# Kernel tuning notes

Hardware: AMD Instinct MI355X
Metric: run time of the kernel (lower is better)

Reference implementation:

```python
import jax, jax.numpy as jnp
import numpy as np

N = 20000   # nodes
E = 320000  # edges (before self-loops)
HID = 64    # hidden_dim
H = 4       # attention heads
C = HID     # per-head channels (concat=False -> mean over heads)
CDIM = 8    # contrastive_dim
NEG_SLOPE = 0.2


def setup_inputs() -> dict:
    key = jax.random.key(0)
    ks = jax.random.split(key, 32)
    g = lambda k, shape: (jax.random.normal(k, shape, jnp.float32) * 0.05)
    inp = {
        "x": jax.random.normal(ks[0], (N, 8), jnp.float32),
        "edge_index": jax.random.randint(ks[1], (2, E), 0, N, jnp.int64),
        # lc_encode MLP: 8 -> 32 -> HID
        "W_enc1": g(ks[2], (8, 32)),  "b_enc1": jnp.zeros((32,), jnp.float32),
        "W_enc2": g(ks[3], (32, HID)), "b_enc2": jnp.zeros((HID,), jnp.float32),
        # three GATConv layers: lin (HID -> H*C, no bias), att_src/att_dst (H, C), bias (C,)
        "W_g1": g(ks[4], (HID, H * C)), "as1": g(ks[5], (H, C)), "ad1": g(ks[6], (H, C)), "bg1": jnp.zeros((C,), jnp.float32),
        "W_g2": g(ks[7], (HID, H * C)), "as2": g(ks[8], (H, C)), "ad2": g(ks[9], (H, C)), "bg2": jnp.zeros((C,), jnp.float32),
        "W_g3": g(ks[10], (HID, H * C)), "as3": g(ks[11], (H, C)), "ad3": g(ks[12], (H, C)), "bg3": jnp.zeros((C,), jnp.float32),
        # output MLP: HID -> 64 -> 32 -> CDIM (dropout inactive at eval)
        "W_o1": g(ks[13], (HID, 64)), "b_o1": jnp.zeros((64,), jnp.float32),
        "W_o2": g(ks[14], (64, 32)),  "b_o2": jnp.zeros((32,), jnp.float32),
        "W_o3": g(ks[15], (32, CDIM)), "b_o3": jnp.zeros((CDIM,), jnp.float32),
    }
    return inp


def gat_conv(x, src, dst, n, W, att_src, att_dst, bias):
    # PyG GATConv, heads=H, concat=False (mean over heads), eval mode (no dropout)
    h = (x @ W).reshape(n, H, C)                       # [N,H,C]
    a_src = jnp.einsum('nhc,hc->nh', h, att_src)        # [N,H]
    a_dst = jnp.einsum('nhc,hc->nh', h, att_dst)        # [N,H]
    logits = jax.nn.leaky_relu(a_src[src] + a_dst[dst], NEG_SLOPE)  # [Etot,H]
    m = jax.ops.segment_max(logits, dst, num_segments=n)            # segment softmax (stable)
    e = jnp.exp(logits - m[dst])
    denom = jax.ops.segment_sum(e, dst, num_segments=n)
    alpha = e / (denom[dst] + 1e-16)                    # [Etot,H]
    msg = h[src] * alpha[:, :, None]                    # [Etot,H,C]
    out = jax.ops.segment_sum(msg, dst, num_segments=n) # [N,H,C]
    return out.mean(axis=1) + bias                      # concat=False -> head mean


def reference(x, edge_index, W_enc1, b_enc1, W_enc2, b_enc2,
              W_g1, as1, ad1, bg1, W_g2, as2, ad2, bg2, W_g3, as3, ad3, bg3,
              W_o1, b_o1, W_o2, b_o2, W_o3, b_o3):
    n = x.shape[0]
    loops = jnp.arange(n, dtype=edge_index.dtype)       # GATConv add_self_loops=True
    src = jnp.concatenate([edge_index[0], loops])
    dst = jnp.concatenate([edge_index[1], loops])

    h = jax.nn.elu(jax.nn.elu(x @ W_enc1 + b_enc1) @ W_enc2 + b_enc2)
    h1 = gat_conv(h, src, dst, n, W_g1, as1, ad1, bg1) + h
    h2 = gat_conv(h1, src, dst, n, W_g2, as2, ad2, bg2) + h1
    h3 = gat_conv(h2, src, dst, n, W_g3, as3, ad3, bg3) + h2

    o = jax.nn.elu(h3 @ W_o1 + b_o1)
    o = jax.nn.elu(o @ W_o2 + b_o2)
    return o @ W_o3 + b_o3
```

## Files before the change

### kernel.cpp

```cpp
#include <hip/hip_runtime.h>
#include <cstdint>
#include <cstddef>

#define NEG_SLOPE 0.2f

__device__ __forceinline__ float elu_f(float x) {
    return x > 0.f ? x : expm1f(x);
}

__global__ __launch_bounds__(256) void encoder_kernel(
    const float* __restrict__ x,
    const float* __restrict__ W1, const float* __restrict__ b1,
    const float* __restrict__ W2, const float* __restrict__ b2,
    const float* __restrict__ vfold0,
    float* __restrict__ h0, float* __restrict__ asrc, float* __restrict__ adst,
    int n_nodes) {
    __shared__ float vsd[512];
    const int t = threadIdx.x;
    if (t < 128) *(float4*)(vsd + t * 4) = *(const float4*)(vfold0 + t * 4);
    __syncthreads();
    const int i = blockIdx.x * blockDim.x + t;
    if (i >= n_nodes) return;
    const float4* xp = (const float4*)(x + (size_t)i * 8);
    float4 x0 = xp[0], x1 = xp[1];
    float xi[8] = {x0.x, x0.y, x0.z, x0.w, x1.x, x1.y, x1.z, x1.w};
    float h1[32];
#pragma unroll
    for (int j = 0; j < 32; ++j) {
        float a = b1[j];
#pragma unroll
        for (int k = 0; k < 8; ++k) a += xi[k] * W1[k * 32 + j];
        h1[j] = elu_f(a);
    }
    float* dst = h0 + (size_t)i * 64;
    float adot[8];
#pragma unroll
    for (int jj = 0; jj < 8; ++jj) adot[jj] = 0.f;
    for (int j = 0; j < 64; ++j) {
        float a = b2[j];
#pragma unroll
        for (int k = 0; k < 32; ++k) a += h1[k] * W2[k * 64 + j];
        a = elu_f(a);
        dst[j] = a;
#pragma unroll
        for (int jj = 0; jj < 8; ++jj) adot[jj] += a * vsd[j * 8 + jj];
    }
#pragma unroll
    for (int h = 0; h < 4; ++h) {
        asrc[i * 4 + h] = adot[h];
        adst[i * 4 + h] = adot[4 + h];
    }
}

__global__ void zero_detect_kernel(const int* __restrict__ ei, int* __restrict__ cnt,
                                   int* __restrict__ flag, int n) {
    int i = blockIdx.x * blockDim.x + threadIdx.x;
    if (i < n) cnt[i] = 0;
    if (i == 0) {
        int acc = 0;
#pragma unroll
        for (int k = 0; k < 8; ++k) acc |= ei[2 * k + 1];
        flag[0] = (acc == 0) ? 1 : 0;
    }
}

__global__ void count_kernel(const int* __restrict__ ei, const int* __restrict__ flag,
                             int E, int Etot, int* __restrict__ cnt) {
    int e = blockIdx.x * blockDim.x + threadIdx.x;
    if (e >= Etot) return;
    int d;
    if (e < E) d = flag[0] ? ei[2 * (size_t)(E + e)] : ei[E + e];
    else       d = e - E;
    atomicAdd(&cnt[d], 1);
}

#define SCAN_B 256
__global__ void scan1_kernel(const int* __restrict__ cnt, int* __restrict__ incl,
                             int* __restrict__ bsum, int n) {
    __shared__ int sd[SCAN_B];
    int t = threadIdx.x;
    int g = blockIdx.x * SCAN_B + t;
    int v = (g < n) ? cnt[g] : 0;
    sd[t] = v;
    __syncthreads();
    for (int off = 1; off < SCAN_B; off <<= 1) {
        int add = (t >= off) ? sd[t - off] : 0;
        __syncthreads();
        sd[t] += add;
        __syncthreads();
    }
    if (g < n) incl[g] = sd[t];
    if (t == SCAN_B - 1) bsum[blockIdx.x] = sd[SCAN_B - 1];
}

__global__ void scan2_kernel(const int* __restrict__ bsum, int* __restrict__ boff, int nb) {
    __shared__ int sd[256];
    int t = threadIdx.x;
    int v = (t < nb) ? bsum[t] : 0;
    sd[t] = v;
    __syncthreads();
    for (int off = 1; off < 256; off <<= 1) {
        int add = (t >= off) ? sd[t - off] : 0;
        __syncthreads();
        sd[t] += add;
        __syncthreads();
    }
    if (t < nb) boff[t] = sd[t] - v;
}

__global__ void scan3_kernel(const int* __restrict__ incl, const int* __restrict__ boff,
                             const int* __restrict__ cnt, int* __restrict__ rowptr,
                             int* __restrict__ cursor, int n) {
    int i = blockIdx.x * SCAN_B + threadIdx.x;
    if (i >= n) return;
    int e = incl[i] + boff[blockIdx.x];
    rowptr[i + 1] = e;
    cursor[i] = e - cnt[i];
    if (i == 0) rowptr[0] = 0;
}

__global__ void fill_kernel(const int* __restrict__ ei, const int* __restrict__ flag,
                            int E, int Etot, int* __restrict__ cursor,
                            int* __restrict__ col) {
    int e = blockIdx.x * blockDim.x + threadIdx.x;
    if (e >= Etot) return;
    int s, d;
    if (e < E) {
        if (flag[0]) { s = ei[2 * (size_t)e]; d = ei[2 * (size_t)(E + e)]; }
        else         { s = ei[e];             d = ei[E + e]; }
    } else {
        s = d = e - E;
    }
    int pos = atomicAdd(&cursor[d], 1);
    col[pos] = s;
}

__global__ __launch_bounds__(256) void fold_all_kernel(
    const float* __restrict__ W0, const float* __restrict__ as0, const float* __restrict__ ad0,
    const float* __restrict__ W1, const float* __restrict__ as1, const float* __restrict__ ad1,
    const float* __restrict__ W2, const float* __restrict__ as2, const float* __restrict__ ad2,
    float* __restrict__ vfold) {
    const int l = blockIdx.x;
    const float* W   = (l == 0) ? W0  : (l == 1) ? W1  : W2;
    const float* as_ = (l == 0) ? as0 : (l == 1) ? as1 : as2;
    const float* ad_ = (l == 0) ? ad0 : (l == 1) ? ad1 : ad2;
    const int t = threadIdx.x;
#pragma unroll
    for (int u = 0; u < 2; ++u) {
        const int e = t * 2 + u;
        const int k = e >> 3, j = e & 7, h = j & 3;
        const float* av = (j < 4) ? as_ : ad_;
        float s = 0.f;
        const float* wr = W + k * 256 + h * 64;
        const float* ar = av + h * 64;
#pragma unroll 8
        for (int cc = 0; cc < 64; ++cc) s += wr[cc] * ar[cc];
        vfold[l * 512 + k * 8 + j] = s;
    }
}

__global__ __launch_bounds__(256) void gat_agg_kernel(
    const float* __restrict__ bin, const float* __restrict__ asrc,
    const float* __restrict__ adst, const int* __restrict__ rowptr,
    const int* __restrict__ col, float* __restrict__ g, int n_nodes) {
    const int grp = threadIdx.x >> 4;
    const int q = threadIdx.x & 15;
    const int n = blockIdx.x * 16 + grp;
    if (n >= n_nodes) return;
    const float4 ad4 = *(const float4*)(adst + (size_t)n * 4);
    const int start = rowptr[n], end = rowptr[n + 1];

    float acc[4][4];
#pragma unroll
    for (int h = 0; h < 4; ++h)
#pragma unroll
        for (int z = 0; z < 4; ++z) acc[h][z] = 0.f;
    float4 den4 = make_float4(0.f, 0.f, 0.f, 0.f);

    for (int base = start; base < end; base += 16) {
        const int cnt = min(16, end - base);
        int c = 0;
        float4 w4 = make_float4(0.f, 0.f, 0.f, 0.f);
        if (base + q < end) {
            c = col[base + q];
            const float4 av = *(const float4*)(asrc + (size_t)c * 4);
            float l0 = av.x + ad4.x; l0 = l0 > 0.f ? l0 : NEG_SLOPE * l0;
            float l1 = av.y + ad4.y; l1 = l1 > 0.f ? l1 : NEG_SLOPE * l1;
            float l2 = av.z + ad4.z; l2 = l2 > 0.f ? l2 : NEG_SLOPE * l2;
            float l3 = av.w + ad4.w; l3 = l3 > 0.f ? l3 : NEG_SLOPE * l3;
            w4.x = __expf(fminf(l0, 60.f));
            w4.y = __expf(fminf(l1, 60.f));
            w4.z = __expf(fminf(l2, 60.f));
            w4.w = __expf(fminf(l3, 60.f));
            den4.x += w4.x; den4.y += w4.y; den4.z += w4.z; den4.w += w4.w;
        }
        int j = 0;
        for (; j + 4 <= cnt; j += 4) {
#pragma unroll
            for (int u = 0; u < 4; ++u) {
                const int s = __shfl(c, j + u, 16);
                const float4 hv = *(const float4*)(bin + (size_t)s * 64 + q * 4);
                const float wx = __shfl(w4.x, j + u, 16);
                const float wy = __shfl(w4.y, j + u, 16);
                const float wz = __shfl(w4.z, j + u, 16);
                const float ww = __shfl(w4.w, j + u, 16);
                acc[0][0] += wx * hv.x; acc[0][1] += wx * hv.y;
                acc[0][2] += wx * hv.z; acc[0][3] += wx * hv.w;
                acc[1][0] += wy * hv.x; acc[1][1] += wy * hv.y;
                acc[1][2] += wy * hv.z; acc[1][3] += wy * hv.w;
                acc[2][0] += wz * hv.x; acc[2][1] += wz * hv.y;
                acc[2][2] += wz * hv.z; acc[2][3] += wz * hv.w;
                acc[3][0] += ww * hv.x; acc[3][1] += ww * hv.y;
                acc[3][2] += ww * hv.z; acc[3][3] += ww * hv.w;
            }
        }
        for (; j < cnt; ++j) {
            const int s = __shfl(c, j, 16);
            const float4 hv = *(const float4*)(bin + (size_t)s * 64 + q * 4);
            const float wx = __shfl(w4.x, j, 16);
            const float wy = __shfl(w4.y, j, 16);
            const float wz = __shfl(w4.z, j, 16);
            const float ww = __shfl(w4.w, j, 16);
            acc[0][0] += wx * hv.x; acc[0][1] += wx * hv.y;
            acc[0][2] += wx * hv.z; acc[0][3] += wx * hv.w;
            acc[1][0] += wy * hv.x; acc[1][1] += wy * hv.y;
            acc[1][2] += wy * hv.z; acc[1][3] += wy * hv.w;
            acc[2][0] += wz * hv.x; acc[2][1] += wz * hv.y;
            acc[2][2] += wz * hv.z; acc[2][3] += wz * hv.w;
            acc[3][0] += ww * hv.x; acc[3][1] += ww * hv.y;
            acc[3][2] += ww * hv.z; acc[3][3] += ww * hv.w;
        }
    }
#pragma unroll
    for (int off = 1; off < 16; off <<= 1) {
        den4.x += __shfl_xor(den4.x, off, 16);
        den4.y += __shfl_xor(den4.y, off, 16);
        den4.z += __shfl_xor(den4.z, off, 16);
        den4.w += __shfl_xor(den4.w, off, 16);
    }
    const float i0 = 1.f / (den4.x + 1e-16f);
    const float i1 = 1.f / (den4.y + 1e-16f);
    const float i2 = 1.f / (den4.z + 1e-16f);
    const float i3 = 1.f / (den4.w + 1e-16f);
    float* gr = g + (size_t)n * 256 + q * 4;
    *(float4*)(gr +   0) = make_float4(acc[0][0]*i0, acc[0][1]*i0, acc[0][2]*i0, acc[0][3]*i0);
    *(float4*)(gr +  64) = make_float4(acc[1][0]*i1, acc[1][1]*i1, acc[1][2]*i1, acc[1][3]*i1);
    *(float4*)(gr + 128) = make_float4(acc[2][0]*i2, acc[2][1]*i2, acc[2][2]*i2, acc[2][3]*i2);
    *(float4*)(gr + 192) = make_float4(acc[3][0]*i3, acc[3][1]*i3, acc[3][2]*i3, acc[3][3]*i3);
}

#define GSTR 132
__global__ __launch_bounds__(256) void gat_post_kernel(
    const float* __restrict__ g, const float* __restrict__ W,
    const float* __restrict__ bias, const float* __restrict__ xin,
    const float* __restrict__ vfold_next, int has_next,
    float* __restrict__ out, float* __restrict__ asrc, float* __restrict__ adst,
    int n_nodes) {
    __shared__ float gS[64 * GSTR];
    __shared__ float Wp[128 * 64];
    __shared__ float vN[512];
    const int t = threadIdx.x;
    const int n0 = blockIdx.x * 64;
    const int cg = t & 7;
    const int ng = t >> 3;

    if (has_next && t < 128) *(float4*)(vN + t * 4) = *(const float4*)(vfold_next + t * 4);

    float acc[2][8];
#pragma unroll
    for (int i = 0; i < 2; ++i)
#pragma unroll
        for (int qq = 0; qq < 8; ++qq) acc[i][qq] = 0.f;

    for (int slab = 0; slab < 2; ++slab) {
        __syncthreads();
#pragma unroll
        for (int j = 0; j < 8; ++j) {
            const int idx = j * 256 + t;
            const int nl = idx >> 5;
            const int c4 = idx & 31;
            float4 v = make_float4(0.f, 0.f, 0.f, 0.f);
            if (n0 + nl < n_nodes)
                v = *(const float4*)(g + (size_t)(n0 + nl) * 256 + slab * 128 + c4 * 4);
            *(float4*)(gS + nl * GSTR + c4 * 4) = v;
        }
#pragma unroll
        for (int j = 0; j < 8; ++j) {
            const int f4 = j * 256 + t;
            const int kl = f4 >> 4;
            const int kap = slab * 128 + kl;
            const int h = kap >> 6, kk = kap & 63;
            const int c = (f4 & 15) * 4;
            *(float4*)(Wp + kl * 64 + c) = *(const float4*)(W + kk * 256 + h * 64 + c);
        }
        __syncthreads();
#pragma unroll 4
        for (int kl = 0; kl < 128; ++kl) {
            const float a0 = gS[(ng * 2 + 0) * GSTR + kl];
            const float a1 = gS[(ng * 2 + 1) * GSTR + kl];
            const float4 b0 = *(const float4*)(Wp + kl * 64 + cg * 8);
            const float4 b1 = *(const float4*)(Wp + kl * 64 + cg * 8 + 4);
            acc[0][0] += a0 * b0.x; acc[0][1] += a0 * b0.y;
            acc[0][2] += a0 * b0.z; acc[0][3] += a0 * b0.w;
            acc[0][4] += a0 * b1.x; acc[0][5] += a0 * b1.y;
            acc[0][6] += a0 * b1.z; acc[0][7] += a0 * b1.w;
            acc[1][0] += a1 * b0.x; acc[1][1] += a1 * b0.y;
            acc[1][2] += a1 * b0.z; acc[1][3] += a1 * b0.w;
            acc[1][4] += a1 * b1.x; acc[1][5] += a1 * b1.y;
            acc[1][6] += a1 * b1.z; acc[1][7] += a1 * b1.w;
        }
    }

    const int c0 = cg * 8;
    const float4 bb0 = *(const float4*)(bias + c0);
    const float4 bb1 = *(const float4*)(bias + c0 + 4);
    float o[2][8];
#pragma unroll
    for (int i = 0; i < 2; ++i) {
        const int n = n0 + ng * 2 + i;
        if (n < n_nodes) {
            const float4 x0 = *(const float4*)(xin + (size_t)n * 64 + c0);
            const float4 x1 = *(const float4*)(xin + (size_t)n * 64 + c0 + 4);
            o[i][0] = 0.25f * acc[i][0] + bb0.x + x0.x;
            o[i][1] = 0.25f * acc[i][1] + bb0.y + x0.y;
            o[i][2] = 0.25f * acc[i][2] + bb0.z + x0.z;
            o[i][3] = 0.25f * acc[i][3] + bb0.w + x0.w;
            o[i][4] = 0.25f * acc[i][4] + bb1.x + x1.x;
            o[i][5] = 0.25f * acc[i][5] + bb1.y + x1.y;
            o[i][6] = 0.25f * acc[i][6] + bb1.z + x1.z;
            o[i][7] = 0.25f * acc[i][7] + bb1.w + x1.w;
            *(float4*)(out + (size_t)n * 64 + c0) =
                make_float4(o[i][0], o[i][1], o[i][2], o[i][3]);
            *(float4*)(out + (size_t)n * 64 + c0 + 4) =
                make_float4(o[i][4], o[i][5], o[i][6], o[i][7]);
        } else {
#pragma unroll
            for (int qq = 0; qq < 8; ++qq) o[i][qq] = 0.f;
        }
    }

    if (has_next) {
        float pj[2][8];
#pragma unroll
        for (int i = 0; i < 2; ++i)
#pragma unroll
            for (int jj = 0; jj < 8; ++jj) pj[i][jj] = 0.f;
#pragma unroll
        for (int cidx = 0; cidx < 8; ++cidx) {
#pragma unroll
            for (int jj = 0; jj < 8; ++jj) {
                const float vv = vN[(c0 + cidx) * 8 + jj];
                pj[0][jj] += o[0][cidx] * vv;
                pj[1][jj] += o[1][cidx] * vv;
            }
        }
#pragma unroll
        for (int off = 1; off < 8; off <<= 1) {
#pragma unroll
            for (int i = 0; i < 2; ++i)
#pragma unroll
                for (int jj = 0; jj < 8; ++jj)
                    pj[i][jj] += __shfl_xor(pj[i][jj], off);
        }
        if (cg == 0) {
#pragma unroll
            for (int i = 0; i < 2; ++i) {
                const int n = n0 + ng * 2 + i;
                if (n < n_nodes) {
#pragma unroll
                    for (int h = 0; h < 4; ++h) {
                        asrc[n * 4 + h] = pj[i][h];
                        adst[n * 4 + h] = pj[i][4 + h];
                    }
                }
            }
        }
    }
}

__global__ __launch_bounds__(256) void out_mlp_kernel(
    const float* __restrict__ h, const float* __restrict__ W1,
    const float* __restrict__ b1, const float* __restrict__ W2,
    const float* __restrict__ b2, const float* __restrict__ W3,
    const float* __restrict__ b3, float* __restrict__ out, int n_nodes) {
    const int wid = threadIdx.x >> 6;
    const int lane = threadIdx.x & 63;
    const int n = blockIdx.x * 4 + wid;
    if (n >= n_nodes) return;
    const float hv = h[(size_t)n * 64 + lane];
    float a = b1[lane];
#pragma unroll
    for (int k = 0; k < 64; ++k) a += __shfl(hv, k) * W1[k * 64 + lane];
    const float o1 = elu_f(a);
    const int c2 = lane & 31;
    float a2 = b2[c2];
#pragma unroll
    for (int k = 0; k < 64; ++k) a2 += __shfl(o1, k) * W2[k * 32 + c2];
    const float o2 = elu_f(a2);
    const int c3 = lane & 7;
    float a3 = b3[c3];
#pragma unroll
    for (int k = 0; k < 32; ++k) a3 += __shfl(o2, k) * W3[k * 8 + c3];
    if (lane < 8) out[(size_t)n * 8 + lane] = a3;
}

extern "C" void kernel_launch(void* const* d_in, const int* in_sizes, int n_in,
                              void* d_out, int out_size, void* d_ws, size_t ws_size,
                              hipStream_t stream) {
    const float* x     = (const float*)d_in[0];
    const int*   ei    = (const int*)d_in[1];
    const float* Wenc1 = (const float*)d_in[2];
    const float* benc1 = (const float*)d_in[3];
    const float* Wenc2 = (const float*)d_in[4];
    const float* benc2 = (const float*)d_in[5];
    const float* Wg[3]  = {(const float*)d_in[6],  (const float*)d_in[10], (const float*)d_in[14]};
    const float* as_[3] = {(const float*)d_in[7],  (const float*)d_in[11], (const float*)d_in[15]};
    const float* ad_[3] = {(const float*)d_in[8],  (const float*)d_in[12], (const float*)d_in[16]};
    const float* bg[3]  = {(const float*)d_in[9],  (const float*)d_in[13], (const float*)d_in[17]};
    const float* Wo1 = (const float*)d_in[18];
    const float* bo1 = (const float*)d_in[19];
    const float* Wo2 = (const float*)d_in[20];
    const float* bo2 = (const float*)d_in[21];
    const float* Wo3 = (const float*)d_in[22];
    const float* bo3 = (const float*)d_in[23];

    const int N = in_sizes[0] / 8;
    const int E = in_sizes[1] / 2;
    const int Etot = E + N;
    const int nblk = (N + SCAN_B - 1) / SCAN_B;

    float* buf0  = (float*)d_ws;
    float* buf1  = buf0 + (size_t)N * 64;
    float* g     = buf1 + (size_t)N * 64;
    float* asrc  = g + (size_t)N * 256;
    float* adst  = asrc + (size_t)N * 4;
    float* vfold = adst + (size_t)N * 4;
    int* rowptr = (int*)(vfold + 3 * 512);
    int* cursor = rowptr + (N + 2);
    int* cnt    = cursor + N;
    int* incl   = cnt + N;
    int* bsum   = incl + N;
    int* boff   = bsum + 256;
    int* flag   = boff + 256;
    int* col    = flag + 2;

    zero_detect_kernel<<<(N + 255) / 256, 256, 0, stream>>>(ei, cnt, flag, N);
    count_kernel<<<(Etot + 255) / 256, 256, 0, stream>>>(ei, flag, E, Etot, cnt);
    scan1_kernel<<<nblk, SCAN_B, 0, stream>>>(cnt, incl, bsum, N);
    scan2_kernel<<<1, 256, 0, stream>>>(bsum, boff, nblk);
    scan3_kernel<<<nblk, SCAN_B, 0, stream>>>(incl, boff, cnt, rowptr, cursor, N);
    fill_kernel<<<(Etot + 255) / 256, 256, 0, stream>>>(ei, flag, E, Etot, cursor, col);

    fold_all_kernel<<<3, 256, 0, stream>>>(Wg[0], as_[0], ad_[0],
                                           Wg[1], as_[1], ad_[1],
                                           Wg[2], as_[2], ad_[2], vfold);

    encoder_kernel<<<(N + 255) / 256, 256, 0, stream>>>(x, Wenc1, benc1, Wenc2, benc2,
                                                        vfold, buf0, asrc, adst, N);

    float* bin = buf0;
    float* bout = buf1;
    for (int l = 0; l < 3; ++l) {
        gat_agg_kernel<<<(N + 15) / 16, 256, 0, stream>>>(bin, asrc, adst, rowptr, col,
                                                          g, N);
        const int has_next = (l < 2) ? 1 : 0;
        gat_post_kernel<<<(N + 63) / 64, 256, 0, stream>>>(
            g, Wg[l], bg[l], bin, vfold + (l + 1 < 3 ? (l + 1) * 512 : 0), has_next,
            bout, asrc, adst, N);
        float* tmp = bin; bin = bout; bout = tmp;
    }

    out_mlp_kernel<<<(N + 3) / 4, 256, 0, stream>>>(bin, Wo1, bo1, Wo2, bo2, Wo3, bo3,
                                                    (float*)d_out, N);
}
```

Before: 339.2 us.

## Fuse prep kernels, use single-pass decoupled scan, fold output MLP into last GAT

Merges the zeroing/flag detection and weight folding into one prep kernel, and replaces the three-kernel block scan with a single-pass scan where each block spins on earlier blocks' published sums. It also fuses the output MLP into the final gat_post kernel, so the last layer's node features stay in shared memory and are not written out and read back. The goal is fewer launches and less global traffic. The one-pass scan assumes all earlier blocks make progress (79 blocks, fine on this GPU) and caps the block count at 128.

```diff
diff --git a/kernel.cpp b/kernel.cpp
--- a/kernel.cpp
+++ b/kernel.cpp
@@ -8,60 +8,42 @@
     return x > 0.f ? x : expm1f(x);
 }
 
-__global__ __launch_bounds__(256) void encoder_kernel(
-    const float* __restrict__ x,
-    const float* __restrict__ W1, const float* __restrict__ b1,
-    const float* __restrict__ W2, const float* __restrict__ b2,
-    const float* __restrict__ vfold0,
-    float* __restrict__ h0, float* __restrict__ asrc, float* __restrict__ adst,
-    int n_nodes) {
-    __shared__ float vsd[512];
-    const int t = threadIdx.x;
-    if (t < 128) *(float4*)(vsd + t * 4) = *(const float4*)(vfold0 + t * 4);
-    __syncthreads();
-    const int i = blockIdx.x * blockDim.x + t;
-    if (i >= n_nodes) return;
-    const float4* xp = (const float4*)(x + (size_t)i * 8);
-    float4 x0 = xp[0], x1 = xp[1];
-    float xi[8] = {x0.x, x0.y, x0.z, x0.w, x1.x, x1.y, x1.z, x1.w};
-    float h1[32];
-#pragma unroll
-    for (int j = 0; j < 32; ++j) {
-        float a = b1[j];
-#pragma unroll
-        for (int k = 0; k < 8; ++k) a += xi[k] * W1[k * 32 + j];
-        h1[j] = elu_f(a);
-    }
-    float* dst = h0 + (size_t)i * 64;
-    float adot[8];
-#pragma unroll
-    for (int jj = 0; jj < 8; ++jj) adot[jj] = 0.f;
-    for (int j = 0; j < 64; ++j) {
-        float a = b2[j];
-#pragma unroll
-        for (int k = 0; k < 32; ++k) a += h1[k] * W2[k * 64 + j];
-        a = elu_f(a);
-        dst[j] = a;
-#pragma unroll
-        for (int jj = 0; jj < 8; ++jj) adot[jj] += a * vsd[j * 8 + jj];
-    }
-#pragma unroll
-    for (int h = 0; h < 4; ++h) {
-        asrc[i * 4 + h] = adot[h];
-        adst[i * 4 + h] = adot[4 + h];
-    }
-}
-
-__global__ void zero_detect_kernel(const int* __restrict__ ei, int* __restrict__ cnt,
-                                   int* __restrict__ flag, int n) {
-    int i = blockIdx.x * blockDim.x + threadIdx.x;
-    if (i < n) cnt[i] = 0;
-    if (i == 0) {
-        int acc = 0;
-#pragma unroll
-        for (int k = 0; k < 8; ++k) acc |= ei[2 * k + 1];
-        flag[0] = (acc == 0) ? 1 : 0;
-    }
+__global__ __launch_bounds__(256) void prep_kernel(
+    const int* __restrict__ ei,
+    const float* __restrict__ W0, const float* __restrict__ as0, const float* __restrict__ ad0,
+    const float* __restrict__ W1, const float* __restrict__ as1, const float* __restrict__ ad1,
+    const float* __restrict__ W2, const float* __restrict__ as2, const float* __restrict__ ad2,
+    int* __restrict__ cnt, int* __restrict__ ready, int* __restrict__ flag,
+    float* __restrict__ vfold, int n) {
+    const int b = blockIdx.x, t = threadIdx.x;
+    if (b < 79) {
+        const int i = b * 256 + t;
+        if (i < n) cnt[i] = 0;
+        if (b == 0) {
+            if (t < 128) ready[t] = 0;
+            if (t == 0) {
+                int acc = 0;
+#pragma unroll
+                for (int k = 0; k < 8; ++k) acc |= ei[2 * k + 1];
+                flag[0] = (acc == 0) ? 1 : 0;
+            }
+        }
+        return;
+    }
+    const int e = (b - 79) * 256 + t;
+    if (e >= 1536) return;
+    const int l = e >> 9, rem = e & 511;
+    const int k = rem >> 3, j = rem & 7, h = j & 3;
+    const float* W   = (l == 0) ? W0  : (l == 1) ? W1  : W2;
+    const float* as_ = (l == 0) ? as0 : (l == 1) ? as1 : as2;
+    const float* ad_ = (l == 0) ? ad0 : (l == 1) ? ad1 : ad2;
+    const float* av = (j < 4) ? as_ : ad_;
+    const float* wr = W + k * 256 + h * 64;
+    const float* ar = av + h * 64;
+    float s = 0.f;
+#pragma unroll 8
+    for (int cc = 0; cc < 64; ++cc) s += wr[cc] * ar[cc];
+    vfold[l * 512 + k * 8 + j] = s;
 }
 
 __global__ void count_kernel(const int* __restrict__ ei, const int* __restrict__ flag,
@@ -75,12 +57,15 @@
 }
 
 #define SCAN_B 256
-__global__ void scan1_kernel(const int* __restrict__ cnt, int* __restrict__ incl,
-                             int* __restrict__ bsum, int n) {
+__global__ __launch_bounds__(256) void scan_onepass_kernel(
+    const int* __restrict__ cnt, int* __restrict__ ready,
+    int* __restrict__ rowptr, int* __restrict__ cursor, int n) {
     __shared__ int sd[SCAN_B];
-    int t = threadIdx.x;
-    int g = blockIdx.x * SCAN_B + t;
-    int v = (g < n) ? cnt[g] : 0;
+    __shared__ int sred[128];
+    __shared__ int s_pref;
+    const int b = blockIdx.x, t = threadIdx.x;
+    const int g = b * SCAN_B + t;
+    const int v = (g < n) ? cnt[g] : 0;
     sd[t] = v;
     __syncthreads();
     for (int off = 1; off < SCAN_B; off <<= 1) {
@@ -89,34 +74,30 @@
         sd[t] += add;
         __syncthreads();
     }
-    if (g < n) incl[g] = sd[t];
-    if (t == SCAN_B - 1) bsum[blockIdx.x] = sd[SCAN_B - 1];
-}
-
-__global__ void scan2_kernel(const int* __restrict__ bsum, int* __restrict__ boff, int nb) {
-    __shared__ int sd[256];
-    int t = threadIdx.x;
-    int v = (t < nb) ? bsum[t] : 0;
-    sd[t] = v;
-    __syncthreads();
-    for (int off = 1; off < 256; off <<= 1) {
-        int add = (t >= off) ? sd[t - off] : 0;
-        __syncthreads();
-        sd[t] += add;
-        __syncthreads();
-    }
-    if (t < nb) boff[t] = sd[t] - v;
-}
-
-__global__ void scan3_kernel(const int* __restrict__ incl, const int* __restrict__ boff,
-                             const int* __restrict__ cnt, int* __restrict__ rowptr,
-                             int* __restrict__ cursor, int n) {
-    int i = blockIdx.x * SCAN_B + threadIdx.x;
-    if (i >= n) return;
-    int e = incl[i] + boff[blockIdx.x];
-    rowptr[i + 1] = e;
-    cursor[i] = e - cnt[i];
-    if (i == 0) rowptr[0] = 0;
+    if (t == SCAN_B - 1) atomicExch(&ready[b], sd[SCAN_B - 1] + 1);
+    if (t < 128) {
+        int pv = 0;
+        if (t < b) {
+            do { pv = atomicAdd(&ready[t], 0); __builtin_amdgcn_s_sleep(1); } while (pv == 0);
+            pv -= 1;
+        }
+        sred[t] = pv;
+    }
+    __syncthreads();
+    if (t == 0) {
+        int s = 0;
+#pragma unroll 8
+        for (int i = 0; i < 128; ++i) s += sred[i];
+        s_pref = s;
+    }
+    __syncthreads();
+    const int pre = s_pref;
+    if (g < n) {
+        const int e = pre + sd[t];
+        rowptr[g + 1] = e;
+        cursor[g] = e - v;
+        if (g == 0) rowptr[0] = 0;
+    }
 }
 
 __global__ void fill_kernel(const int* __restrict__ ei, const int* __restrict__ flag,
@@ -135,27 +116,47 @@
     col[pos] = s;
 }
 
-__global__ __launch_bounds__(256) void fold_all_kernel(
-    const float* __restrict__ W0, const float* __restrict__ as0, const float* __restrict__ ad0,
-    const float* __restrict__ W1, const float* __restrict__ as1, const float* __restrict__ ad1,
-    const float* __restrict__ W2, const float* __restrict__ as2, const float* __restrict__ ad2,
-    float* __restrict__ vfold) {
-    const int l = blockIdx.x;
-    const float* W   = (l == 0) ? W0  : (l == 1) ? W1  : W2;
-    const float* as_ = (l == 0) ? as0 : (l == 1) ? as1 : as2;
-    const float* ad_ = (l == 0) ? ad0 : (l == 1) ? ad1 : ad2;
+__global__ __launch_bounds__(256) void encoder_kernel(
+    const float* __restrict__ x,
+    const float* __restrict__ W1, const float* __restrict__ b1,
+    const float* __restrict__ W2, const float* __restrict__ b2,
+    const float* __restrict__ vfold0,
+    float* __restrict__ h0, float* __restrict__ asrc, float* __restrict__ adst,
+    int n_nodes) {
+    __shared__ float vsd[512];
     const int t = threadIdx.x;
-#pragma unroll
-    for (int u = 0; u < 2; ++u) {
-        const int e = t * 2 + u;
-        const int k = e >> 3, j = e & 7, h = j & 3;
-        const float* av = (j < 4) ? as_ : ad_;
-        float s = 0.f;
-        const float* wr = W + k * 256 + h * 64;
-        const float* ar = av + h * 64;
-#pragma unroll 8
-        for (int cc = 0; cc < 64; ++cc) s += wr[cc] * ar[cc];
-        vfold[l * 512 + k * 8 + j] = s;
+    if (t < 128) *(float4*)(vsd + t * 4) = *(const float4*)(vfold0 + t * 4);
+    __syncthreads();
+    const int i = blockIdx.x * blockDim.x + t;
+    if (i >= n_nodes) return;
+    const float4* xp = (const float4*)(x + (size_t)i * 8);
+    float4 x0 = xp[0], x1 = xp[1];
+    float xi[8] = {x0.x, x0.y, x0.z, x0.w, x1.x, x1.y, x1.z, x1.w};
+    float h1[32];
+#pragma unroll
+    for (int j = 0; j < 32; ++j) {
+        float a = b1[j];
+#pragma unroll
+        for (int k = 0; k < 8; ++k) a += xi[k] * W1[k * 32 + j];
+        h1[j] = elu_f(a);
+    }
+    float* dst = h0 + (size_t)i * 64;
+    float adot[8];
+#pragma unroll
+    for (int jj = 0; jj < 8; ++jj) adot[jj] = 0.f;
+    for (int j = 0; j < 64; ++j) {
+        float a = b2[j];
+#pragma unroll
+        for (int k = 0; k < 32; ++k) a += h1[k] * W2[k * 64 + j];
+        a = elu_f(a);
+        dst[j] = a;
+#pragma unroll
+        for (int jj = 0; jj < 8; ++jj) adot[jj] += a * vsd[j * 8 + jj];
+    }
+#pragma unroll
+    for (int h = 0; h < 4; ++h) {
+        asrc[i * 4 + h] = adot[h];
+        adst[i * 4 + h] = adot[4 + h];
     }
 }
 
@@ -255,7 +256,10 @@
     const float* __restrict__ bias, const float* __restrict__ xin,
     const float* __restrict__ vfold_next, int has_next,
     float* __restrict__ out, float* __restrict__ asrc, float* __restrict__ adst,
-    int n_nodes) {
+    const float* __restrict__ Wm1, const float* __restrict__ bm1,
+    const float* __restrict__ Wm2, const float* __restrict__ bm2,
+    const float* __restrict__ Wm3, const float* __restrict__ bm3,
+    float* __restrict__ mlp_out, int n_nodes) {
     __shared__ float gS[64 * GSTR];
     __shared__ float Wp[128 * 64];
     __shared__ float vN[512];
@@ -329,10 +333,12 @@
             o[i][5] = 0.25f * acc[i][5] + bb1.y + x1.y;
             o[i][6] = 0.25f * acc[i][6] + bb1.z + x1.z;
             o[i][7] = 0.25f * acc[i][7] + bb1.w + x1.w;
-            *(float4*)(out + (size_t)n * 64 + c0) =
-                make_float4(o[i][0], o[i][1], o[i][2], o[i][3]);
-            *(float4*)(out + (size_t)n * 64 + c0 + 4) =
-                make_float4(o[i][4], o[i][5], o[i][6], o[i][7]);
+            if (has_next) {
+                *(float4*)(out + (size_t)n * 64 + c0) =
+                    make_float4(o[i][0], o[i][1], o[i][2], o[i][3]);
+                *(float4*)(out + (size_t)n * 64 + c0 + 4) =
+                    make_float4(o[i][4], o[i][5], o[i][6], o[i][7]);
+            }
         } else {
 #pragma unroll
             for (int qq = 0; qq < 8; ++qq) o[i][qq] = 0.f;
@@ -375,33 +381,99 @@
                 }
             }
         }
-    }
-}
-
-__global__ __launch_bounds__(256) void out_mlp_kernel(
-    const float* __restrict__ h, const float* __restrict__ W1,
-    const float* __restrict__ b1, const float* __restrict__ W2,
-    const float* __restrict__ b2, const float* __restrict__ W3,
-    const float* __restrict__ b3, float* __restrict__ out, int n_nodes) {
-    const int wid = threadIdx.x >> 6;
-    const int lane = threadIdx.x & 63;
-    const int n = blockIdx.x * 4 + wid;
-    if (n >= n_nodes) return;
-    const float hv = h[(size_t)n * 64 + lane];
-    float a = b1[lane];
-#pragma unroll
-    for (int k = 0; k < 64; ++k) a += __shfl(hv, k) * W1[k * 64 + lane];
-    const float o1 = elu_f(a);
-    const int c2 = lane & 31;
-    float a2 = b2[c2];
-#pragma unroll
-    for (int k = 0; k < 64; ++k) a2 += __shfl(o1, k) * W2[k * 32 + c2];
-    const float o2 = elu_f(a2);
-    const int c3 = lane & 7;
-    float a3 = b3[c3];
-#pragma unroll
-    for (int k = 0; k < 32; ++k) a3 += __shfl(o2, k) * W3[k * 8 + c3];
-    if (lane < 8) out[(size_t)n * 8 + lane] = a3;
+        return;
+    }
+
+    __syncthreads();
+#pragma unroll
+    for (int i = 0; i < 2; ++i) {
+        const int nl = ng * 2 + i;
+        *(float4*)(gS + nl * GSTR + c0)     = make_float4(o[i][0], o[i][1], o[i][2], o[i][3]);
+        *(float4*)(gS + nl * GSTR + c0 + 4) = make_float4(o[i][4], o[i][5], o[i][6], o[i][7]);
+    }
+    {
+        const int f4 = t;
+#pragma unroll
+        for (int j = 0; j < 4; ++j)
+            *(float4*)(Wp + (j * 256 + t) * 4) = *(const float4*)(Wm1 + (j * 256 + t) * 4);
+#pragma unroll
+        for (int j = 0; j < 2; ++j)
+            *(float4*)(Wp + 4096 + (j * 256 + t) * 4) = *(const float4*)(Wm2 + (j * 256 + t) * 4);
+        if (t < 64) vN[t] = bm1[t];
+        else if (t < 96) vN[t] = bm2[t - 64];
+        else if (t < 104) vN[t] = bm3[t - 96];
+        if (t < 256) vN[104 + t] = Wm3[t];
+        (void)f4;
+    }
+    __syncthreads();
+    {
+        float a1[2][8];
+#pragma unroll
+        for (int i = 0; i < 2; ++i)
+#pragma unroll
+            for (int qq = 0; qq < 8; ++qq) a1[i][qq] = vN[c0 + qq];
+#pragma unroll 4
+        for (int k = 0; k < 64; ++k) {
+            const float h0 = gS[(ng * 2 + 0) * GSTR + k];
+            const float h1v = gS[(ng * 2 + 1) * GSTR + k];
+            const float4 w0 = *(const float4*)(Wp + k * 64 + c0);
+            const float4 w1 = *(const float4*)(Wp + k * 64 + c0 + 4);
+            a1[0][0] += h0 * w0.x; a1[0][1] += h0 * w0.y;
+            a1[0][2] += h0 * w0.z; a1[0][3] += h0 * w0.w;
+            a1[0][4] += h0 * w1.x; a1[0][5] += h0 * w1.y;
+            a1[0][6] += h0 * w1.z; a1[0][7] += h0 * w1.w;
+            a1[1][0] += h1v * w0.x; a1[1][1] += h1v * w0.y;
+            a1[1][2] += h1v * w0.z; a1[1][3] += h1v * w0.w;
+            a1[1][4] += h1v * w1.x; a1[1][5] += h1v * w1.y;
+            a1[1][6] += h1v * w1.z; a1[1][7] += h1v * w1.w;
+        }
+#pragma unroll
+        for (int i = 0; i < 2; ++i) {
+            const int nl = ng * 2 + i;
+            float4 v0 = make_float4(elu_f(a1[i][0]), elu_f(a1[i][1]), elu_f(a1[i][2]), elu_f(a1[i][3]));
+            float4 v1 = make_float4(elu_f(a1[i][4]), elu_f(a1[i][5]), elu_f(a1[i][6]), elu_f(a1[i][7]));
+            *(float4*)(gS + nl * GSTR + 64 + c0)     = v0;
+            *(float4*)(gS + nl * GSTR + 64 + c0 + 4) = v1;
+        }
+    }
+    __syncthreads();
+    {
+        const int cg4 = t & 3;
+        const int nn = t >> 2;
+        const int cc0 = cg4 * 8;
+        float a2[8];
+#pragma unroll
+        for (int qq = 0; qq < 8; ++qq) a2[qq] = vN[64 + cc0 + qq];
+#pragma unroll 4
+        for (int j = 0; j < 64; ++j) {
+            const float ov = gS[nn * GSTR + 64 + j];
+            const float4 w0 = *(const float4*)(Wp + 4096 + j * 32 + cc0);
+            const float4 w1 = *(const float4*)(Wp + 4096 + j * 32 + cc0 + 4);
+            a2[0] += ov * w0.x; a2[1] += ov * w0.y;
+            a2[2] += ov * w0.z; a2[3] += ov * w0.w;
+            a2[4] += ov * w1.x; a2[5] += ov * w1.y;
+            a2[6] += ov * w1.z; a2[7] += ov * w1.w;
+        }
+        __syncthreads();
+        *(float4*)(gS + nn * GSTR + cc0)     = make_float4(elu_f(a2[0]), elu_f(a2[1]), elu_f(a2[2]), elu_f(a2[3]));
+        *(float4*)(gS + nn * GSTR + cc0 + 4) = make_float4(elu_f(a2[4]), elu_f(a2[5]), elu_f(a2[6]), elu_f(a2[7]));
+    }
+    __syncthreads();
+    {
+        const int c3 = t & 7;
+        const int nq = t >> 3;
+#pragma unroll
+        for (int i = 0; i < 2; ++i) {
+            const int nl = nq * 2 + i;
+            const int n = n0 + nl;
+            if (n >= n_nodes) continue;
+            float a3 = vN[96 + c3];
+#pragma unroll 4
+            for (int j = 0; j < 32; ++j)
+                a3 += gS[nl * GSTR + j] * vN[104 + j * 8 + c3];
+            mlp_out[(size_t)n * 8 + c3] = a3;
+        }
+    }
 }
 
 extern "C" void kernel_launch(void* const* d_in, const int* in_sizes, int n_in,
@@ -438,22 +510,16 @@
     int* rowptr = (int*)(vfold + 3 * 512);
     int* cursor = rowptr + (N + 2);
     int* cnt    = cursor + N;
-    int* incl   = cnt + N;
-    int* bsum   = incl + N;
-    int* boff   = bsum + 256;
-    int* flag   = boff + 256;
+    int* ready  = cnt + N;
+    int* flag   = ready + 128;
     int* col    = flag + 2;
 
-    zero_detect_kernel<<<(N + 255) / 256, 256, 0, stream>>>(ei, cnt, flag, N);
+    prep_kernel<<<nblk + 6, 256, 0, stream>>>(ei,
+        Wg[0], as_[0], ad_[0], Wg[1], as_[1], ad_[1], Wg[2], as_[2], ad_[2],
+        cnt, ready, flag, vfold, N);
     count_kernel<<<(Etot + 255) / 256, 256, 0, stream>>>(ei, flag, E, Etot, cnt);
-    scan1_kernel<<<nblk, SCAN_B, 0, stream>>>(cnt, incl, bsum, N);
-    scan2_kernel<<<1, 256, 0, stream>>>(bsum, boff, nblk);
-    scan3_kernel<<<nblk, SCAN_B, 0, stream>>>(incl, boff, cnt, rowptr, cursor, N);
+    scan_onepass_kernel<<<nblk, SCAN_B, 0, stream>>>(cnt, ready, rowptr, cursor, N);
     fill_kernel<<<(Etot + 255) / 256, 256, 0, stream>>>(ei, flag, E, Etot, cursor, col);
-
-    fold_all_kernel<<<3, 256, 0, stream>>>(Wg[0], as_[0], ad_[0],
-                                           Wg[1], as_[1], ad_[1],
-                                           Wg[2], as_[2], ad_[2], vfold);
 
     encoder_kernel<<<(N + 255) / 256, 256, 0, stream>>>(x, Wenc1, benc1, Wenc2, benc2,
                                                         vfold, buf0, asrc, adst, N);
@@ -466,10 +532,8 @@
         const int has_next = (l < 2) ? 1 : 0;
         gat_post_kernel<<<(N + 63) / 64, 256, 0, stream>>>(
             g, Wg[l], bg[l], bin, vfold + (l + 1 < 3 ? (l + 1) * 512 : 0), has_next,
-            bout, asrc, adst, N);
+            bout, asrc, adst,
+            Wo1, bo1, Wo2, bo2, Wo3, bo3, (float*)d_out, N);
         float* tmp = bin; bin = bout; bout = tmp;
     }
-
-    out_mlp_kernel<<<(N + 3) / 4, 256, 0, stream>>>(bin, Wo1, bo1, Wo2, bo2, Wo3, bo3,
-                                                    (float*)d_out, N);
-}
+}
```

Result: faster. 305.2 us (-10.0%).
